# Kernel tuning notes

Hardware: AMD Instinct MI355X
Metric: run time of the kernel (lower is better)

The kernel has to match this reference:

```python
import jax, jax.numpy as jnp
import numpy as np

N, E, D, H, Z, HEADS = 20000, 160000, 3000, 512, 50, 3
EPS = 1e-5


def _bn(x, gamma, beta):
    # BatchNorm1d, training-mode stats (biased variance), eps=1e-5
    m = x.mean(axis=0)
    v = x.var(axis=0)
    return (x - m) * jax.lax.rsqrt(v + EPS) * gamma + beta


def _gat(x, src, dst, n, W, att_src, att_dst, bias, heads, c):
    # PyG GATConv, concat=False (mean over heads), negative_slope=0.2
    h = (x @ W).reshape(n, heads, c)                      # [N,H,C]
    a_s = (h * att_src).sum(-1)                           # [N,H]
    a_d = (h * att_dst).sum(-1)                           # [N,H]
    e = jax.nn.leaky_relu(a_s[src] + a_d[dst], 0.2)       # [Etot,H]
    e = e - jax.ops.segment_max(e, dst, num_segments=n)[dst]
    ex = jnp.exp(e)
    den = jax.ops.segment_sum(ex, dst, num_segments=n)[dst]
    alpha = ex / den                                      # segment softmax over incoming edges
    msg = h[src] * alpha[:, :, None]                      # [Etot,H,C]
    out = jax.ops.segment_sum(msg, dst, num_segments=n)   # [N,H,C]
    return out.mean(axis=1) + bias


def setup_inputs() -> dict:
    key = jax.random.key(0)
    ks = jax.random.split(key, 16)
    s = 0.05
    inp = {
        "x": jax.random.normal(ks[0], (N, D), dtype=jnp.float32),
        "edge_index": jax.random.randint(ks[1], (2, E), 0, N, dtype=jnp.int64),
        "W1": jax.random.normal(ks[2], (D, HEADS * H), dtype=jnp.float32) * s,
        "att_src1": jax.random.normal(ks[3], (HEADS, H), dtype=jnp.float32) * s,
        "att_dst1": jax.random.normal(ks[4], (HEADS, H), dtype=jnp.float32) * s,
        "b1": jnp.zeros((H,), jnp.float32),
        "bn1_g": jnp.ones((H,), jnp.float32),
        "bn1_b": jnp.zeros((H,), jnp.float32),
        "W2": jax.random.normal(ks[5], (H, HEADS * Z), dtype=jnp.float32) * s,
        "att_src2": jax.random.normal(ks[6], (HEADS, Z), dtype=jnp.float32) * s,
        "att_dst2": jax.random.normal(ks[7], (HEADS, Z), dtype=jnp.float32) * s,
        "b2": jnp.zeros((Z,), jnp.float32),
        "bn2_g": jnp.ones((Z,), jnp.float32),
        "bn2_b": jnp.zeros((Z,), jnp.float32),
        "lin1_w": jax.random.normal(ks[8], (H, Z), dtype=jnp.float32) * s,
        "lin1_b": jnp.zeros((H,), jnp.float32),
        "dbn_g": jnp.ones((H,), jnp.float32),
        "dbn_b": jnp.zeros((H,), jnp.float32),
        "lin2_w": jax.random.normal(ks[9], (D, H), dtype=jnp.float32) * s,
        "lin2_b": jnp.zeros((D,), jnp.float32),
    }
    return inp


def reference(x, edge_index, W1, att_src1, att_dst1, b1, bn1_g, bn1_b,
              W2, att_src2, att_dst2, b2, bn2_g, bn2_b,
              lin1_w, lin1_b, dbn_g, dbn_b, lin2_w, lin2_b):
    n = x.shape[0]
    loop = jnp.arange(n, dtype=edge_index.dtype)
    src = jnp.concatenate([edge_index[0], loop])  # add self-loops (PyG default)
    dst = jnp.concatenate([edge_index[1], loop])
    h = jax.nn.relu(_bn(_gat(x, src, dst, n, W1, att_src1, att_dst1, b1, HEADS, H), bn1_g, bn1_b))
    z = jax.nn.relu(_bn(_gat(h, src, dst, n, W2, att_src2, att_dst2, b2, HEADS, Z), bn2_g, bn2_b))
    d = jax.nn.relu(_bn(z @ lin1_w.T + lin1_b, dbn_g, dbn_b))
    out = jax.nn.relu(d @ lin2_w.T + lin2_b)
    return out
```

## Files before the change

### kernel.cpp

```cpp
#include <hip/hip_runtime.h>
#include <stdint.h>

typedef unsigned short u16;
typedef __attribute__((ext_vector_type(8))) short s16x8;
typedef __attribute__((ext_vector_type(4))) short s16x4;
typedef __attribute__((ext_vector_type(4))) float f32x4;

#define DEVFN static __device__ __forceinline__

static constexpr int NN = 20000;
static constexpr int EE = 160000;
static constexpr int ET = 180000;
static constexpr int DD = 3000;
static constexpr int HH = 512;
static constexpr int ZZ = 50;
static constexpr int C1 = 1536;
static constexpr int C2 = 150;
static constexpr int KA1 = 3008;
static constexpr int KP1 = 3072;

DEVFN u16 f2b(float f) {
  uint32_t u = __builtin_bit_cast(uint32_t, f);
  u += 0x7FFFu + ((u >> 16) & 1u);
  return (u16)(u >> 16);
}
DEVFN float b2f(u16 b) {
  uint32_t u = ((uint32_t)b) << 16;
  return __builtin_bit_cast(float, u);
}
DEVFN int edge_at(const void* ei, int mode32, long idx) {
  return mode32 ? ((const int*)ei)[idx] : (int)((const long long*)ei)[idx];
}

typedef __attribute__((address_space(1))) const unsigned int gas_uint;
typedef __attribute__((address_space(3))) unsigned int las_uint;
DEVFN void async16(const u16* g, u16* l) {
  __builtin_amdgcn_global_load_lds((gas_uint*)(uintptr_t)g,
                                   (las_uint*)(unsigned)(uintptr_t)l, 16, 0, 0);
}

DEVFN int sniff_mode(const void* ei, int* nzsh) {
  if (threadIdx.x == 0) *nzsh = 0;
  __syncthreads();
  const int* e32 = (const int*)ei;
  int loc = 0;
  for (int i = threadIdx.x; i < 1024; i += blockDim.x)
    if (e32[2 * i + 1] != 0) loc = 1;
  if (loc) atomicOr(nzsh, 1);
  __syncthreads();
  return *nzsh;
}

__global__ void k_deg(const void* ei, int* __restrict__ deg) {
  __shared__ int nz;
  int m = sniff_mode(ei, &nz);
  long i = (long)blockIdx.x * blockDim.x + threadIdx.x;
  long st = (long)gridDim.x * blockDim.x;
  for (; i < ET; i += st) {
    int d = (i < EE) ? edge_at(ei, m, EE + i) : (int)(i - EE);
    if ((unsigned)d < (unsigned)NN) atomicAdd(&deg[d], 1);
  }
}

__global__ void k_scan_blk(int* __restrict__ deg, int* __restrict__ rowptr,
                           int* __restrict__ bsum) {
  __shared__ int buf[256];
  int b = blockIdx.x, tid = threadIdx.x;
  int i = b * 256 + tid;
  buf[tid] = (i < NN) ? deg[i] : 0;
  if (i < NN) deg[i] = 0;
  __syncthreads();
  for (int off = 1; off < 256; off <<= 1) {
    int t = (tid >= off) ? buf[tid - off] : 0;
    __syncthreads();
    buf[tid] += t;
    __syncthreads();
  }
  if (i < NN) rowptr[i + 1] = buf[tid];
  if (tid == 255) bsum[b] = buf[255];
}
__global__ void k_scan_top(int* __restrict__ bsum, int nb) {
  __shared__ int buf[128];
  int tid = threadIdx.x;
  buf[tid] = (tid < nb) ? bsum[tid] : 0;
  __syncthreads();
  for (int off = 1; off < 128; off <<= 1) {
    int t = (tid >= off) ? buf[tid - off] : 0;
    __syncthreads();
    buf[tid] += t;
    __syncthreads();
  }
  if (tid < nb) bsum[tid] = buf[tid];
}
__global__ void k_scan_add(int* __restrict__ rowptr, const int* __restrict__ bsum) {
  int b = blockIdx.x, tid = threadIdx.x;
  int i = b * 256 + tid;
  if (i == 0) rowptr[0] = 0;
  if (b > 0 && i < NN) rowptr[i + 1] += bsum[b - 1];
}

__global__ void k_fill(const void* ei, const int* __restrict__ rowptr,
                       int* __restrict__ cursor, int* __restrict__ srcp) {
  __shared__ int nz;
  int m = sniff_mode(ei, &nz);
  long i = (long)blockIdx.x * blockDim.x + threadIdx.x;
  long st = (long)gridDim.x * blockDim.x;
  for (; i < ET; i += st) {
    int s, d;
    if (i < EE) { s = edge_at(ei, m, i); d = edge_at(ei, m, EE + i); }
    else { s = d = (int)(i - EE); }
    if ((unsigned)d < (unsigned)NN && (unsigned)s < (unsigned)NN) {
      int pos = atomicAdd(&cursor[d], 1);
      srcp[rowptr[d] + pos] = s;
    }
  }
}

__global__ void k_cvt_pad4(const float* __restrict__ in, u16* __restrict__ out,
                           int R, int Cin, int ldo) {
  int r = blockIdx.y;
  int c = (blockIdx.x * blockDim.x + threadIdx.x) * 4;
  if (c >= ldo) return;
  s16x4 o;
  const float* src = in + (size_t)r * Cin + c;
  if (r < R && c + 4 <= Cin && ((((size_t)r * Cin + c) & 3) == 0)) {
    f32x4 v = *(const f32x4*)src;
#pragma unroll
    for (int j = 0; j < 4; j++) o[j] = (short)f2b(v[j]);
  } else {
#pragma unroll
    for (int j = 0; j < 4; j++)
      o[j] = (short)((r < R && c + j < Cin) ? f2b(src[j]) : (u16)0);
  }
  *(s16x4*)(out + (size_t)r * ldo + c) = o;
}

__global__ void k_transpose_tile(const float* __restrict__ in, u16* __restrict__ out,
                                 int R, int Cc, int ldo) {
  __shared__ float t[32][33];
  int tx = threadIdx.x & 31, ty = threadIdx.x >> 5;
  int c0 = blockIdx.x * 32, r0 = blockIdx.y * 32;
#pragma unroll
  for (int j = 0; j < 4; j++) {
    int r = r0 + ty + j * 8, c = c0 + tx;
    t[ty + j * 8][tx] = (r < R && c < Cc) ? in[(size_t)r * Cc + c] : 0.f;
  }
  __syncthreads();
#pragma unroll
  for (int j = 0; j < 4; j++) {
    int c = c0 + ty + j * 8, r = r0 + tx;
    if (c < Cc && r < ldo) out[(size_t)c * ldo + r] = f2b(t[tx][ty + j * 8]);
  }
}

__global__ void k_transpose_cvt2(const float* __restrict__ in, u16* __restrict__ out,
                                 int R, int C, int Cp, int ldo) {
  long total = (long)Cp * ldo;
  long i = (long)blockIdx.x * blockDim.x + threadIdx.x;
  long st = (long)gridDim.x * blockDim.x;
  for (; i < total; i += st) {
    int c = (int)(i / ldo), r = (int)(i % ldo);
    out[i] = (c < C && r < R) ? f2b(in[(size_t)r * C + c]) : (u16)0;
  }
}

template<bool OUT_BF16, bool RELU>
__global__ __launch_bounds__(512, 2) void k_gemm8(
    const u16* __restrict__ Ag, const u16* __restrict__ Bg, void* __restrict__ Cg,
    const float* __restrict__ bias, int M, int Nn, int Kp, int lda, int ldb, int ldc) {
  __shared__ __align__(16) u16 As[2][256][64];
  __shared__ __align__(16) u16 Bs[2][256][64];
  int tid = threadIdx.x;
  int lane = tid & 63, wid = tid >> 6;
  int wm = wid >> 2, wn = wid & 3;
  int lr = lane & 15, lg = lane >> 4;
  int rx = lr & 7;

  int nwg = gridDim.x * gridDim.y;
  int wg = blockIdx.y * gridDim.x + blockIdx.x;
  int q = nwg >> 3, r = nwg & 7;
  int xcd = wg & 7, loc = wg >> 3;
  int swz = (xcd < r ? xcd * (q + 1) : r * (q + 1) + (xcd - r) * q) + loc;
  int m0 = (swz / gridDim.x) * 256, n0 = (swz % gridDim.x) * 256;

  int srow = tid >> 3;
  int schunk = ((tid & 7) ^ (srow & 7)) * 8;
  const u16* agp[4];
  const u16* bgp[4];
#pragma unroll
  for (int i = 0; i < 4; i++) {
    int ra = i * 64 + srow;
    int ga = m0 + ra; if (ga > M - 1) ga = M - 1;
    agp[i] = Ag + (size_t)ga * lda + schunk;
    bgp[i] = Bg + (size_t)(n0 + ra) * ldb + schunk;
  }
  u16* aB0 = &As[0][0][0]; u16* aB1 = &As[1][0][0];
  u16* bB0 = &Bs[0][0][0]; u16* bB1 = &Bs[1][0][0];

#define SA(cb, h, kt) do {                                                  \
    u16* d_ = ((cb) ? aB1 : aB0);                                           \
    async16(agp[2*(h)]   + (size_t)(kt)*64, d_ + (2*(h))*4096 + wid*512);   \
    async16(agp[2*(h)+1] + (size_t)(kt)*64, d_ + (2*(h)+1)*4096 + wid*512); \
  } while (0)
#define SB(cb, h, kt) do {                                                  \
    u16* d_ = ((cb) ? bB1 : bB0);                                           \
    async16(bgp[2*(h)]   + (size_t)(kt)*64, d_ + (2*(h))*4096 + wid*512);   \
    async16(bgp[2*(h)+1] + (size_t)(kt)*64, d_ + (2*(h)+1)*4096 + wid*512); \
  } while (0)
#define BARX() do { asm volatile("" ::: "memory");                          \
    __builtin_amdgcn_s_barrier(); asm volatile("" ::: "memory"); } while (0)
#define VMC4() asm volatile("s_waitcnt vmcnt(4)" ::: "memory")
#define RDA(dst, cb, mi, ks) dst = *(const s16x8*)&As[cb][wm*128+(mi)*16+lr][(((ks)*4+lg)^rx)*8]
#define RDB(dst, cb, ni, ks) dst = *(const s16x8*)&Bs[cb][wn*64+(ni)*16+lr][(((ks)*4+lg)^rx)*8]

  f32x4 acc[8][4];
#pragma unroll
  for (int mi = 0; mi < 8; mi++)
#pragma unroll
    for (int ni = 0; ni < 4; ni++) {
      acc[mi][ni][0] = 0.f; acc[mi][ni][1] = 0.f;
      acc[mi][ni][2] = 0.f; acc[mi][ni][3] = 0.f;
    }

  s16x8 bfr[2][4];
  s16x8 f0[4], f1[4];

#define RDB8(cb) do {                                                   \
    RDB(bfr[0][0], cb, 0, 0); RDB(bfr[0][1], cb, 1, 0);                 \
    RDB(bfr[0][2], cb, 2, 0); RDB(bfr[0][3], cb, 3, 0);                 \
    RDB(bfr[1][0], cb, 0, 1); RDB(bfr[1][1], cb, 1, 1);                 \
    RDB(bfr[1][2], cb, 2, 1); RDB(bfr[1][3], cb, 3, 1); } while (0)
#define RDAP(F, cb, P) do {                                             \
    RDA(F[0], cb, 2*(P), 0);   RDA(F[1], cb, 2*(P), 1);                 \
    RDA(F[2], cb, 2*(P)+1, 0); RDA(F[3], cb, 2*(P)+1, 1); } while (0)
#define DO_MFMA(P, F) do {                                              \
    _Pragma("unroll")                                                   \
    for (int ni_ = 0; ni_ < 4; ni_++) {                                 \
      acc[2*(P)][ni_]   = __builtin_amdgcn_mfma_f32_16x16x32_bf16(F[0], bfr[0][ni_], acc[2*(P)][ni_], 0, 0, 0);   \
      acc[2*(P)][ni_]   = __builtin_amdgcn_mfma_f32_16x16x32_bf16(F[1], bfr[1][ni_], acc[2*(P)][ni_], 0, 0, 0);   \
      acc[2*(P)+1][ni_] = __builtin_amdgcn_mfma_f32_16x16x32_bf16(F[2], bfr[0][ni_], acc[2*(P)+1][ni_], 0, 0, 0); \
      acc[2*(P)+1][ni_] = __builtin_amdgcn_mfma_f32_16x16x32_bf16(F[3], bfr[1][ni_], acc[2*(P)+1][ni_], 0, 0, 0); \
    } } while (0)

#define GROUP(cb, S1, S2, S3, S4) do {                                  \
    RDB8(cb); RDAP(f0, cb, 0);                                          \
    S1; BARX();                                                         \
    __builtin_amdgcn_s_setprio(1);                                      \
    RDAP(f1, cb, 1); DO_MFMA(0, f0);                                    \
    __builtin_amdgcn_s_setprio(0);                                      \
    S2; BARX();                                                         \
    __builtin_amdgcn_s_setprio(1);                                      \
    RDAP(f0, cb, 2); DO_MFMA(1, f1);                                    \
    __builtin_amdgcn_s_setprio(0);                                      \
    S3; BARX();                                                         \
    __builtin_amdgcn_s_setprio(1);                                      \
    RDAP(f1, cb, 3); DO_MFMA(2, f0);                                    \
    __builtin_amdgcn_s_setprio(0);                                      \
    S4; BARX();                                                         \
    __builtin_amdgcn_s_setprio(1);                                      \
    DO_MFMA(3, f1);                                                     \
    __builtin_amdgcn_s_setprio(0); VMC4(); BARX();                      \
  } while (0)

  int nt = Kp >> 6;
  SB(0, 0, 0); SB(0, 1, 0);
  SA(0, 0, 0); SA(0, 1, 0);
  { int k1 = 1 < nt ? 1 : nt - 1; SB(1, 0, k1); SB(1, 1, k1); }
  VMC4();
  BARX();

  for (int t = 0; t < nt; t += 2) {
    int t2 = (t + 2 < nt) ? t + 2 : nt - 1;
    int t3 = (t + 3 < nt) ? t + 3 : nt - 1;
    GROUP(0, SA(1, 0, t + 1), SA(1, 1, t + 1), SB(0, 0, t2), SB(0, 1, t2));
    GROUP(1, SA(0, 0, t2),    SA(0, 1, t2),    SB(1, 0, t3), SB(1, 1, t3));
  }
  asm volatile("s_waitcnt vmcnt(0)" ::: "memory");

#undef SA
#undef SB
#undef BARX
#undef VMC4
#undef RDA
#undef RDB
#undef RDB8
#undef RDAP
#undef DO_MFMA
#undef GROUP

#pragma unroll
  for (int mi = 0; mi < 8; mi++)
#pragma unroll
    for (int ni = 0; ni < 4; ni++) {
      int col = n0 + wn * 64 + ni * 16 + lr;
      if (col >= Nn) continue;
      float bv = bias ? bias[col] : 0.f;
#pragma unroll
      for (int j = 0; j < 4; j++) {
        int row = m0 + wm * 128 + mi * 16 + lg * 4 + j;
        if (row >= M) continue;
        float v = acc[mi][ni][j] + bv;
        if (RELU) v = v > 0.f ? v : 0.f;
        if (OUT_BF16) ((u16*)Cg)[(size_t)row * ldc + col] = f2b(v);
        else          ((float*)Cg)[(size_t)row * ldc + col] = v;
      }
    }
}

template<bool OUT_BF16, bool RELU>
__global__ __launch_bounds__(256) void k_gemm3(
    const u16* __restrict__ Ag, const u16* __restrict__ Bg, void* __restrict__ Cg,
    const float* __restrict__ bias, int M, int Nn, int Kp, int ld, int ldc) {
  __shared__ __align__(16) u16 As[2][128][64];
  __shared__ __align__(16) u16 Bs[2][128][64];
  int tid = threadIdx.x;
  int lane = tid & 63, wid = tid >> 6;
  int wm = wid >> 1, wn = wid & 1;
  int lr = lane & 15, lg = lane >> 4;

  int nwg = gridDim.x * gridDim.y;
  int wg = blockIdx.y * gridDim.x + blockIdx.x;
  int q = nwg >> 3, r = nwg & 7;
  int xcd = wg & 7, loc = wg >> 3;
  int swz = (xcd < r ? xcd * (q + 1) : r * (q + 1) + (xcd - r) * q) + loc;
  int m0 = (swz / gridDim.x) * 128, n0 = (swz % gridDim.x) * 128;

  int srow = lane >> 3;
  int skk = ((lane & 7) ^ srow) * 8;
  const u16* agp[4];
  const u16* bgp[4];
#pragma unroll
  for (int i = 0; i < 4; i++) {
    int ra = wid * 32 + i * 8 + srow;
    int ga = m0 + ra; if (ga > M - 1) ga = M - 1;
    agp[i] = Ag + (size_t)ga * ld + skk;
    bgp[i] = Bg + (size_t)(n0 + ra) * ld + skk;
  }

#define STAGE(bufi, kofs) do {                                   \
    u16* la_ = &As[bufi][0][0] + wid * 2048;                     \
    u16* lb_ = &Bs[bufi][0][0] + wid * 2048;                     \
    _Pragma("unroll")                                            \
    for (int i_ = 0; i_ < 4; i_++) {                             \
      async16(agp[i_] + (kofs), la_ + i_ * 512);                 \
      async16(bgp[i_] + (kofs), lb_ + i_ * 512);                 \
    }                                                            \
  } while (0)

  f32x4 acc[4][4];
#pragma unroll
  for (int mi = 0; mi < 4; mi++)
#pragma unroll
    for (int ni = 0; ni < 4; ni++) {
      acc[mi][ni][0] = 0.f; acc[mi][ni][1] = 0.f; acc[mi][ni][2] = 0.f; acc[mi][ni][3] = 0.f;
    }

  int rx = lr & 7;
  int NT = Kp >> 6;
  STAGE(0, 0);
  for (int t = 0; t < NT; t++) {
    int cur = t & 1;
    if (t + 1 < NT) {
      STAGE(cur ^ 1, (t + 1) * 64);
      asm volatile("s_waitcnt vmcnt(8)" ::: "memory");
    } else {
      asm volatile("s_waitcnt vmcnt(0)" ::: "memory");
    }
    __builtin_amdgcn_s_barrier();
    asm volatile("" ::: "memory");
#pragma unroll
    for (int ks = 0; ks < 2; ks++) {
      int ch = ((ks * 4 + lg) ^ rx) * 8;
      s16x8 a[4], b[4];
#pragma unroll
      for (int mi = 0; mi < 4; mi++)
        a[mi] = *(const s16x8*)&As[cur][wm * 64 + mi * 16 + lr][ch];
#pragma unroll
      for (int ni = 0; ni < 4; ni++)
        b[ni] = *(const s16x8*)&Bs[cur][wn * 64 + ni * 16 + lr][ch];
#pragma unroll
      for (int mi = 0; mi < 4; mi++)
#pragma unroll
        for (int ni = 0; ni < 4; ni++)
          acc[mi][ni] = __builtin_amdgcn_mfma_f32_16x16x32_bf16(a[mi], b[ni], acc[mi][ni], 0, 0, 0);
    }
    asm volatile("" ::: "memory");
    __builtin_amdgcn_s_barrier();
  }
#undef STAGE

#pragma unroll
  for (int mi = 0; mi < 4; mi++)
#pragma unroll
    for (int ni = 0; ni < 4; ni++) {
      int col = n0 + wn * 64 + ni * 16 + lr;
      if (col >= Nn) continue;
      float bv = bias ? bias[col] : 0.f;
#pragma unroll
      for (int j = 0; j < 4; j++) {
        int row = m0 + wm * 64 + mi * 16 + lg * 4 + j;
        if (row >= M) continue;
        float v = acc[mi][ni][j] + bv;
        if (RELU) v = v > 0.f ? v : 0.f;
        if (OUT_BF16) ((u16*)Cg)[(size_t)row * ldc + col] = f2b(v);
        else          ((float*)Cg)[(size_t)row * ldc + col] = v;
      }
    }
}

__global__ void k_attdot1b(const u16* __restrict__ h1b, const float* __restrict__ asrc,
                           const float* __restrict__ adst, float* __restrict__ as_,
                           float* __restrict__ ad_, float* __restrict__ z0,
                           float* __restrict__ z1) {
  int n = blockIdx.x;
  if (n == 0) {
    for (int i = threadIdx.x; i < HH; i += 192) { z0[i] = 0.f; z1[i] = 0.f; }
  }
  int hd = threadIdx.x >> 6, lane = threadIdx.x & 63;
  s16x8 h = *(const s16x8*)(h1b + (size_t)n * C1 + hd * 512 + lane * 8);
  const float* ap = asrc + hd * 512 + lane * 8;
  const float* dp = adst + hd * 512 + lane * 8;
  f32x4 a0 = *(const f32x4*)ap, a1 = *(const f32x4*)(ap + 4);
  f32x4 d0 = *(const f32x4*)dp, d1 = *(const f32x4*)(dp + 4);
  float ps = 0.f, pd = 0.f;
#pragma unroll
  for (int j = 0; j < 4; j++) {
    float hv = b2f((u16)h[j]);
    ps += hv * a0[j]; pd += hv * d0[j];
    float hw = b2f((u16)h[j + 4]);
    ps += hw * a1[j]; pd += hw * d1[j];
  }
  for (int off = 32; off; off >>= 1) { ps += __shfl_xor(ps, off); pd += __shfl_xor(pd, off); }
  if (lane == 0) { as_[3 * n + hd] = ps; ad_[3 * n + hd] = pd; }
}

__global__ void k_attdot2(const float* __restrict__ s2, const float* __restrict__ asrc,
                          const float* __restrict__ adst, float* __restrict__ as_,
                          float* __restrict__ ad_, float* __restrict__ z0,
                          float* __restrict__ z1, float* __restrict__ z2,
                          float* __restrict__ z3) {
  int n = blockIdx.x, tid = threadIdx.x;
  if (n == 0) {
    for (int i = tid; i < HH; i += 64) { z2[i] = 0.f; z3[i] = 0.f; }
    if (tid < 50) { z0[tid] = 0.f; z1[tid] = 0.f; }
  }
  for (int hd = 0; hd < 3; hd++) {
    float ps = 0.f, pd = 0.f;
    if (tid < 50) {
      float v = s2[(size_t)n * C2 + hd * 50 + tid];
      ps = v * asrc[hd * 50 + tid];
      pd = v * adst[hd * 50 + tid];
    }
    for (int off = 32; off; off >>= 1) { ps += __shfl_xor(ps, off); pd += __shfl_xor(pd, off); }
    if (tid == 0) { as_[3 * n + hd] = ps; ad_[3 * n + hd] = pd; }
  }
}

__global__ __launch_bounds__(192) void k_gat1(
    const u16* __restrict__ h1b, const float* __restrict__ as1,
    const float* __restrict__ ad1, const int* __restrict__ rowptr,
    const int* __restrict__ srcp, const float* __restrict__ bias,
    float* __restrict__ out) {
  int n = blockIdx.x, tid = threadIdx.x;
  __shared__ float sm[3], sden[3];
  __shared__ int s_src[128];
  __shared__ float s_alpha[128][3];
  __shared__ float part[3][512];
  int r0 = rowptr[n], deg = rowptr[n + 1] - r0;
  float adl[3] = {ad1[3 * n], ad1[3 * n + 1], ad1[3 * n + 2]};

  if (tid < 64) {
    float mx[3] = {-1e30f, -1e30f, -1e30f};
    for (int e = tid; e < deg; e += 64) {
      int s = srcp[r0 + e];
#pragma unroll
      for (int hd = 0; hd < 3; hd++) {
        float v = as1[3 * s + hd] + adl[hd];
        v = v > 0.f ? v : 0.2f * v;
        mx[hd] = fmaxf(mx[hd], v);
      }
    }
#pragma unroll
    for (int hd = 0; hd < 3; hd++)
      for (int off = 32; off; off >>= 1) mx[hd] = fmaxf(mx[hd], __shfl_xor(mx[hd], off));
    float sd[3] = {0.f, 0.f, 0.f};
    for (int e = tid; e < deg; e += 64) {
      int s = srcp[r0 + e];
#pragma unroll
      for (int hd = 0; hd < 3; hd++) {
        float v = as1[3 * s + hd] + adl[hd];
        v = v > 0.f ? v : 0.2f * v;
        sd[hd] += __expf(v - mx[hd]);
      }
    }
#pragma unroll
    for (int hd = 0; hd < 3; hd++)
      for (int off = 32; off; off >>= 1) sd[hd] += __shfl_xor(sd[hd], off);
    if (tid == 0) {
#pragma unroll
      for (int hd = 0; hd < 3; hd++) { sm[hd] = mx[hd]; sden[hd] = sd[hd]; }
    }
  }
  __syncthreads();

  int hd = tid >> 6, lane = tid & 63;
  float a[8];
#pragma unroll
  for (int j = 0; j < 8; j++) a[j] = 0.f;

  for (int base = 0; base < deg; base += 128) {
    int cnt = min(128, deg - base);
    if (tid < cnt) {
      int s = srcp[r0 + base + tid];
      s_src[tid] = s;
#pragma unroll
      for (int h2 = 0; h2 < 3; h2++) {
        float v = as1[3 * s + h2] + adl[h2];
        v = v > 0.f ? v : 0.2f * v;
        s_alpha[tid][h2] = __expf(v - sm[h2]) / sden[h2];
      }
    }
    __syncthreads();
    int e = 0;
    for (; e + 2 <= cnt; e += 2) {
      const u16* p0 = h1b + (size_t)s_src[e] * C1 + (hd << 9) + lane * 8;
      const u16* p1 = h1b + (size_t)s_src[e + 1] * C1 + (hd << 9) + lane * 8;
      s16x8 v0 = *(const s16x8*)p0;
      s16x8 v1 = *(const s16x8*)p1;
      float al0 = s_alpha[e][hd], al1 = s_alpha[e + 1][hd];
#pragma unroll
      for (int j = 0; j < 8; j++)
        a[j] += al0 * b2f((u16)v0[j]) + al1 * b2f((u16)v1[j]);
    }
    if (e < cnt) {
      const u16* p0 = h1b + (size_t)s_src[e] * C1 + (hd << 9) + lane * 8;
      s16x8 v0 = *(const s16x8*)p0;
      float al0 = s_alpha[e][hd];
#pragma unroll
      for (int j = 0; j < 8; j++) a[j] += al0 * b2f((u16)v0[j]);
    }
    __syncthreads();
  }

#pragma unroll
  for (int j = 0; j < 8; j++) part[hd][lane * 8 + j] = a[j];
  __syncthreads();
  if (tid < 128) {
    f32x4 p0 = *(const f32x4*)&part[0][tid * 4];
    f32x4 p1 = *(const f32x4*)&part[1][tid * 4];
    f32x4 p2 = *(const f32x4*)&part[2][tid * 4];
    f32x4 bv = *(const f32x4*)(bias + tid * 4);
    f32x4 o;
#pragma unroll
    for (int j = 0; j < 4; j++) o[j] = (p0[j] + p1[j] + p2[j]) * (1.f / 3.f) + bv[j];
    *(f32x4*)(out + (size_t)n * 512 + tid * 4) = o;
  }
}

__global__ void k_gat2(const float* __restrict__ s2, const float* __restrict__ as2,
                       const float* __restrict__ ad2, const int* __restrict__ rowptr,
                       const int* __restrict__ srcp, const float* __restrict__ bias,
                       float* __restrict__ z) {
  int n = blockIdx.x, tid = threadIdx.x;
  __shared__ int s_src[64];
  __shared__ float s_alpha[64][3];
  int r0 = rowptr[n], deg = rowptr[n + 1] - r0;
  float adl[3] = {ad2[3 * n], ad2[3 * n + 1], ad2[3 * n + 2]};

  float mx[3] = {-1e30f, -1e30f, -1e30f};
  for (int e = tid; e < deg; e += 64) {
    int s = srcp[r0 + e];
#pragma unroll
    for (int hd = 0; hd < 3; hd++) {
      float v = as2[3 * s + hd] + adl[hd];
      v = v > 0.f ? v : 0.2f * v;
      mx[hd] = fmaxf(mx[hd], v);
    }
  }
#pragma unroll
  for (int hd = 0; hd < 3; hd++)
    for (int off = 32; off; off >>= 1) mx[hd] = fmaxf(mx[hd], __shfl_xor(mx[hd], off));
  float sd[3] = {0.f, 0.f, 0.f};
  for (int e = tid; e < deg; e += 64) {
    int s = srcp[r0 + e];
#pragma unroll
    for (int hd = 0; hd < 3; hd++) {
      float v = as2[3 * s + hd] + adl[hd];
      v = v > 0.f ? v : 0.2f * v;
      sd[hd] += __expf(v - mx[hd]);
    }
  }
#pragma unroll
  for (int hd = 0; hd < 3; hd++)
    for (int off = 32; off; off >>= 1) sd[hd] += __shfl_xor(sd[hd], off);

  float acc = 0.f;
  for (int base = 0; base < deg; base += 64) {
    int cnt = min(64, deg - base);
    if (tid < cnt) {
      int s = srcp[r0 + base + tid];
      s_src[tid] = s;
#pragma unroll
      for (int hd = 0; hd < 3; hd++) {
        float v = as2[3 * s + hd] + adl[hd];
        v = v > 0.f ? v : 0.2f * v;
        s_alpha[tid][hd] = __expf(v - mx[hd]) / sd[hd];
      }
    }
    __syncthreads();
    if (tid < 50) {
      for (int e = 0; e < cnt; e++) {
        const float* row = s2 + (size_t)s_src[e] * C2;
#pragma unroll
        for (int hd = 0; hd < 3; hd++) acc += s_alpha[e][hd] * row[hd * 50 + tid];
      }
    }
    __syncthreads();
  }
  if (tid < 50) z[(size_t)n * ZZ + tid] = acc * (1.f / 3.f) + bias[tid];
}

__global__ void k_colstats3(const float* __restrict__ x, float* __restrict__ gsum,
                            float* __restrict__ gsq, long total, int C) {
  long i = (long)blockIdx.x * blockDim.x + threadIdx.x;
  long st = (long)gridDim.x * blockDim.x;
  int c = (int)(i % C);
  float s = 0.f, q = 0.f;
  for (; i < total; i += st) { float v = x[i]; s += v; q += v * v; }
  atomicAdd(&gsum[c], s);
  atomicAdd(&gsq[c], q);
}

__global__ void k_bnrelu4f(const float* __restrict__ x, const float* __restrict__ gsum,
                           const float* __restrict__ gsq, const float* __restrict__ g,
                           const float* __restrict__ bb, u16* __restrict__ out,
                           long total4, float invN) {
  long i = (long)blockIdx.x * blockDim.x + threadIdx.x;
  long st = (long)gridDim.x * blockDim.x;
  for (; i < total4; i += st) {
    long b = i * 4;
    int c = (int)(b & 511);
    f32x4 v = *(const f32x4*)(x + b);
    f32x4 s = *(const f32x4*)(gsum + c);
    f32x4 qv = *(const f32x4*)(gsq + c);
    f32x4 gg = *(const f32x4*)(g + c);
    f32x4 bv = *(const f32x4*)(bb + c);
    s16x4 o;
#pragma unroll
    for (int j = 0; j < 4; j++) {
      float m = s[j] * invN;
      float var = qv[j] * invN - m * m;
      float sc = gg[j] * rsqrtf(var + 1e-5f);
      float r = (v[j] - m) * sc + bv[j];
      r = r > 0.f ? r : 0.f;
      o[j] = (short)f2b(r);
    }
    *(s16x4*)(out + b) = o;
  }
}

__global__ void k_bnrelu_padf(const float* __restrict__ x, const float* __restrict__ gsum,
                              const float* __restrict__ gsq, const float* __restrict__ g,
                              const float* __restrict__ bb, u16* __restrict__ out) {
  int i = blockIdx.x * blockDim.x + threadIdx.x;
  if (i >= NN * 64) return;
  int c = i & 63, r = i >> 6;
  float v = 0.f;
  if (c < 50) {
    float m = gsum[c] * (1.0f / NN);
    float var = gsq[c] * (1.0f / NN) - m * m;
    float sc = g[c] * rsqrtf(var + 1e-5f);
    v = (x[r * 50 + c] - m) * sc + bb[c];
    v = v > 0.f ? v : 0.f;
  }
  out[i] = f2b(v);
}

extern "C" void kernel_launch(void* const* d_in, const int* in_sizes, int n_in,
                              void* d_out, int out_size, void* d_ws, size_t ws_size,
                              hipStream_t stream) {
  (void)in_sizes; (void)n_in; (void)out_size;
  const float* x     = (const float*)d_in[0];
  const void*  ei    = d_in[1];
  const float* W1    = (const float*)d_in[2];
  const float* asrc1 = (const float*)d_in[3];
  const float* adst1 = (const float*)d_in[4];
  const float* b1    = (const float*)d_in[5];
  const float* bn1g  = (const float*)d_in[6];
  const float* bn1b  = (const float*)d_in[7];
  const float* W2    = (const float*)d_in[8];
  const float* asrc2 = (const float*)d_in[9];
  const float* adst2 = (const float*)d_in[10];
  const float* b2    = (const float*)d_in[11];
  const float* bn2g  = (const float*)d_in[12];
  const float* bn2b  = (const float*)d_in[13];
  const float* l1w   = (const float*)d_in[14];
  const float* l1b   = (const float*)d_in[15];
  const float* dbng  = (const float*)d_in[16];
  const float* dbnb  = (const float*)d_in[17];
  const float* l2w   = (const float*)d_in[18];
  const float* l2b   = (const float*)d_in[19];
  float* out = (float*)d_out;
  char* ws = (char*)d_ws;

  size_t off = 0;
  auto alloc = [&](size_t b) { size_t r = off; off += (b + 255) & ~(size_t)255; return r; };
  const size_t oXB  = alloc(120320000);
  const size_t oH1  = alloc(61440000);
  const size_t oW1T = alloc((size_t)C1 * KP1 * 2);
  const size_t oAS1 = alloc((size_t)NN * 12), oAD1 = alloc((size_t)NN * 12);
  const size_t oAS2 = alloc((size_t)NN * 12), oAD2 = alloc((size_t)NN * 12);
  const size_t oRP  = alloc((size_t)(NN + 1) * 4);
  const size_t oDEG = alloc((size_t)NN * 4);
  const size_t oSRC = alloc((size_t)ET * 4);
  const size_t oBSUM = alloc(512);
  const size_t oS1 = alloc(2048), oQ1 = alloc(2048);
  const size_t oS2 = alloc(2048), oQ2 = alloc(2048);
  const size_t oS3 = alloc(2048), oQ3 = alloc(2048);
  if (ws_size < off) return;

  u16*   xb   = (u16*)(ws + oXB);
  float* g1   = (float*)(ws + oXB);
  u16*   h2b  = (u16*)(ws + oXB + 40960000);
  float* s2   = (float*)(ws + oXB + 61440000);
  float* zf   = (float*)(ws + oXB + 73440000);
  u16*   zb   = (u16*)(ws + oXB + 77440000);
  u16*   w2T  = (u16*)(ws + oXB + 80000000);
  u16*   l1wT = (u16*)(ws + oXB + 80262400);
  u16*   l2wT = (u16*)(ws + oXB + 80328192);
  float* dbuf = (float*)(ws + oXB);
  u16*   h1b  = (u16*)(ws + oH1);
  u16*   db   = (u16*)(ws + oH1);
  u16*   w1T  = (u16*)(ws + oW1T);
  int* bsum   = (int*)(ws + oBSUM);
  int* deg    = (int*)(ws + oDEG);
  int* rowptr = (int*)(ws + oRP);
  int* srcp   = (int*)(ws + oSRC);
  float *as1 = (float*)(ws + oAS1), *ad1 = (float*)(ws + oAD1);
  float *as2 = (float*)(ws + oAS2), *ad2 = (float*)(ws + oAD2);
  float *sum1 = (float*)(ws + oS1), *sq1 = (float*)(ws + oQ1);
  float *sum2 = (float*)(ws + oS2), *sq2 = (float*)(ws + oQ2);
  float *sum3 = (float*)(ws + oS3), *sq3 = (float*)(ws + oQ3);

  hipMemsetAsync(deg, 0, (size_t)NN * 4, stream);
  k_deg<<<512, 256, 0, stream>>>(ei, deg);
  k_scan_blk<<<79, 256, 0, stream>>>(deg, rowptr, bsum);
  k_scan_top<<<1, 128, 0, stream>>>(bsum, 79);
  k_scan_add<<<79, 256, 0, stream>>>(rowptr, bsum);
  k_fill<<<512, 256, 0, stream>>>(ei, rowptr, deg, srcp);

  k_cvt_pad4<<<dim3(3, NN), 256, 0, stream>>>(x, xb, NN, DD, KA1);
  k_transpose_tile<<<dim3(C1 / 32, KP1 / 32), 256, 0, stream>>>(W1, w1T, DD, C1, KP1);
  k_gemm8<true, false><<<dim3(6, 79), 512, 0, stream>>>(xb, w1T, h1b, nullptr,
                                                        NN, C1, KP1, KA1, KP1, C1);
  k_attdot1b<<<NN, 192, 0, stream>>>(h1b, asrc1, adst1, as1, ad1, sum1, sq1);
  k_gat1<<<NN, 192, 0, stream>>>(h1b, as1, ad1, rowptr, srcp, b1, g1);
  k_colstats3<<<512, 256, 0, stream>>>(g1, sum1, sq1, (long)NN * HH, HH);
  k_bnrelu4f<<<2048, 256, 0, stream>>>(g1, sum1, sq1, bn1g, bn1b, h2b,
                                       (long)NN * HH / 4, 1.0f / NN);

  k_transpose_cvt2<<<256, 256, 0, stream>>>(W2, w2T, HH, C2, 256, HH);
  k_gemm3<false, false><<<dim3(2, 157), 256, 0, stream>>>(h2b, w2T, s2, nullptr,
                                                          NN, C2, HH, HH, C2);
  k_attdot2<<<NN, 64, 0, stream>>>(s2, asrc2, adst2, as2, ad2, sum2, sq2, sum3, sq3);
  k_gat2<<<NN, 64, 0, stream>>>(s2, as2, ad2, rowptr, srcp, b2, zf);
  k_colstats3<<<25, 256, 0, stream>>>(zf, sum2, sq2, (long)NN * ZZ, ZZ);
  k_bnrelu_padf<<<5000, 256, 0, stream>>>(zf, sum2, sq2, bn2g, bn2b, zb);

  k_cvt_pad4<<<dim3(1, HH), 256, 0, stream>>>(l1w, l1wT, HH, ZZ, 64);
  k_gemm3<false, false><<<dim3(4, 157), 256, 0, stream>>>(zb, l1wT, dbuf, l1b,
                                                          NN, HH, 64, 64, HH);
  k_colstats3<<<512, 256, 0, stream>>>(dbuf, sum3, sq3, (long)NN * HH, HH);
  k_bnrelu4f<<<2048, 256, 0, stream>>>(dbuf, sum3, sq3, dbng, dbnb, db,
                                       (long)NN * HH / 4, 1.0f / NN);
  k_cvt_pad4<<<dim3(1, 3072), 256, 0, stream>>>(l2w, l2wT, DD, HH, HH);
  k_gemm8<false, true><<<dim3(12, 79), 512, 0, stream>>>(db, l2wT, out, l2b,
                                                         NN, DD, 512, HH, HH, DD);
}
```

Before: 716.2 us.

## Fuse fp32-to-bf16 conversion of x into first GEMM's A-tile loads

Removes the separate pass that converts and pads x (20000x3000 fp32) to bf16. The first GEMM now loads fp32 A directly through registers, converts to bf16 and writes it to LDS, with zero-fill past the real K. This saves one full write and one full read of the bf16 copy of x. In exchange, the A path loses async global-to-LDS copies, reads twice the bytes per tile, and adds conversion ALU work and register pressure inside the MFMA loop.

```diff
diff --git a/kernel.cpp b/kernel.cpp
--- a/kernel.cpp
+++ b/kernel.cpp
@@ -16,7 +16,6 @@
 static constexpr int ZZ = 50;
 static constexpr int C1 = 1536;
 static constexpr int C2 = 150;
-static constexpr int KA1 = 3008;
 static constexpr int KP1 = 3072;
 
 DEVFN u16 f2b(float f) {
@@ -164,10 +163,11 @@
   }
 }
 
-template<bool OUT_BF16, bool RELU>
+template<bool OUT_BF16, bool RELU, bool A_F32>
 __global__ __launch_bounds__(512, 2) void k_gemm8(
     const u16* __restrict__ Ag, const u16* __restrict__ Bg, void* __restrict__ Cg,
-    const float* __restrict__ bias, int M, int Nn, int Kp, int lda, int ldb, int ldc) {
+    const float* __restrict__ bias, int M, int Nn, int Kp, int lda, int ldb, int ldc,
+    int Kreal) {
   __shared__ __align__(16) u16 As[2][256][64];
   __shared__ __align__(16) u16 Bs[2][256][64];
   int tid = threadIdx.x;
@@ -186,13 +186,16 @@
   int srow = tid >> 3;
   int schunk = ((tid & 7) ^ (srow & 7)) * 8;
   const u16* agp[4];
+  const float* agf[4];
   const u16* bgp[4];
+  const float* Af = (const float*)Ag;
 #pragma unroll
   for (int i = 0; i < 4; i++) {
-    int ra = i * 64 + srow;
-    int ga = m0 + ra; if (ga > M - 1) ga = M - 1;
+    int ra_ = i * 64 + srow;
+    int ga = m0 + ra_; if (ga > M - 1) ga = M - 1;
     agp[i] = Ag + (size_t)ga * lda + schunk;
-    bgp[i] = Bg + (size_t)(n0 + ra) * ldb + schunk;
+    agf[i] = Af + (size_t)ga * lda + schunk;
+    bgp[i] = Bg + (size_t)(n0 + ra_) * ldb + schunk;
   }
   u16* aB0 = &As[0][0][0]; u16* aB1 = &As[1][0][0];
   u16* bB0 = &Bs[0][0][0]; u16* bB1 = &Bs[1][0][0];
@@ -224,6 +227,37 @@
 
   s16x8 bfr[2][4];
   s16x8 f0[4], f1[4];
+  s16x8 fs[4];
+  f32x4 ra[4];
+
+#define LOADA_F(h, kt) do {                                             \
+    int kk_ = (kt) * 64 + schunk;                                       \
+    _Pragma("unroll")                                                   \
+    for (int j_ = 0; j_ < 2; j_++) {                                    \
+      const float* p_ = agf[2*(h)+j_] + (size_t)(kt) * 64;              \
+      if (kk_ + 8 <= Kreal) {                                           \
+        ra[2*j_]   = *(const f32x4*)p_;                                 \
+        ra[2*j_+1] = *(const f32x4*)(p_ + 4);                           \
+      } else {                                                          \
+        _Pragma("unroll")                                               \
+        for (int e_ = 0; e_ < 4; e_++) {                                \
+          ra[2*j_][e_]   = (kk_ + e_     < Kreal) ? p_[e_]     : 0.f;   \
+          ra[2*j_+1][e_] = (kk_ + 4 + e_ < Kreal) ? p_[e_ + 4] : 0.f;   \
+        }                                                               \
+      }                                                                 \
+    } } while (0)
+#define CVTW_F(buf, h) do {                                             \
+    u16* d_ = ((buf) ? aB1 : aB0);                                      \
+    _Pragma("unroll")                                                   \
+    for (int j_ = 0; j_ < 2; j_++) {                                    \
+      s16x8 o_;                                                         \
+      _Pragma("unroll")                                                 \
+      for (int e_ = 0; e_ < 4; e_++) {                                  \
+        o_[e_]     = (short)f2b(ra[2*j_][e_]);                          \
+        o_[e_ + 4] = (short)f2b(ra[2*j_+1][e_]);                        \
+      }                                                                 \
+      *(s16x8*)(d_ + (2*(h)+j_)*4096 + tid*8) = o_;                     \
+    } } while (0)
 
 #define RDB8(cb) do {                                                   \
     RDB(bfr[0][0], cb, 0, 0); RDB(bfr[0][1], cb, 1, 0);                 \
@@ -262,18 +296,58 @@
     __builtin_amdgcn_s_setprio(0); VMC4(); BARX();                      \
   } while (0)
 
+#define GROUPF(cb, ktA, ktAn, S3, S4) do {                              \
+    RDB8(cb);                                                           \
+    CVTW_F((cb) ^ 1, 0);                                                \
+    LOADA_F(1, ktA);                                                    \
+    RDAP(fs, cb, 0);                                                    \
+    BARX();                                                             \
+    __builtin_amdgcn_s_setprio(1); DO_MFMA(0, fs);                      \
+    __builtin_amdgcn_s_setprio(0);                                      \
+    CVTW_F((cb) ^ 1, 1);                                                \
+    RDAP(fs, cb, 1);                                                    \
+    BARX();                                                             \
+    __builtin_amdgcn_s_setprio(1); DO_MFMA(1, fs);                      \
+    __builtin_amdgcn_s_setprio(0);                                      \
+    S3; RDAP(fs, cb, 2);                                                \
+    BARX();                                                             \
+    __builtin_amdgcn_s_setprio(1); DO_MFMA(2, fs);                      \
+    __builtin_amdgcn_s_setprio(0);                                      \
+    S4; LOADA_F(0, ktAn);                                               \
+    RDAP(fs, cb, 3);                                                    \
+    BARX();                                                             \
+    __builtin_amdgcn_s_setprio(1); DO_MFMA(3, fs);                      \
+    __builtin_amdgcn_s_setprio(0); BARX();                              \
+  } while (0)
+
   int nt = Kp >> 6;
-  SB(0, 0, 0); SB(0, 1, 0);
-  SA(0, 0, 0); SA(0, 1, 0);
-  { int k1 = 1 < nt ? 1 : nt - 1; SB(1, 0, k1); SB(1, 1, k1); }
-  VMC4();
-  BARX();
-
-  for (int t = 0; t < nt; t += 2) {
-    int t2 = (t + 2 < nt) ? t + 2 : nt - 1;
-    int t3 = (t + 3 < nt) ? t + 3 : nt - 1;
-    GROUP(0, SA(1, 0, t + 1), SA(1, 1, t + 1), SB(0, 0, t2), SB(0, 1, t2));
-    GROUP(1, SA(0, 0, t2),    SA(0, 1, t2),    SB(1, 0, t3), SB(1, 1, t3));
+  if constexpr (A_F32) {
+    SB(0, 0, 0); SB(0, 1, 0);
+    LOADA_F(0, 0); CVTW_F(0, 0);
+    LOADA_F(1, 0); CVTW_F(0, 1);
+    int k1 = 1 < nt ? 1 : nt - 1;
+    SB(1, 0, k1); SB(1, 1, k1);
+    LOADA_F(0, k1);
+    asm volatile("s_waitcnt lgkmcnt(0)" ::: "memory");
+    BARX();
+    for (int t = 0; t < nt; t += 2) {
+      int t2 = (t + 2 < nt) ? t + 2 : nt - 1;
+      int t3 = (t + 3 < nt) ? t + 3 : nt - 1;
+      GROUPF(0, t + 1, t2, SB(0, 0, t2), SB(0, 1, t2));
+      GROUPF(1, t2, t3, SB(1, 0, t3), SB(1, 1, t3));
+    }
+  } else {
+    SB(0, 0, 0); SB(0, 1, 0);
+    SA(0, 0, 0); SA(0, 1, 0);
+    { int k1 = 1 < nt ? 1 : nt - 1; SB(1, 0, k1); SB(1, 1, k1); }
+    VMC4();
+    BARX();
+    for (int t = 0; t < nt; t += 2) {
+      int t2 = (t + 2 < nt) ? t + 2 : nt - 1;
+      int t3 = (t + 3 < nt) ? t + 3 : nt - 1;
+      GROUP(0, SA(1, 0, t + 1), SA(1, 1, t + 1), SB(0, 0, t2), SB(0, 1, t2));
+      GROUP(1, SA(0, 0, t2),    SA(0, 1, t2),    SB(1, 0, t3), SB(1, 1, t3));
+    }
   }
   asm volatile("s_waitcnt vmcnt(0)" ::: "memory");
 
@@ -287,6 +361,9 @@
 #undef RDAP
 #undef DO_MFMA
 #undef GROUP
+#undef GROUPF
+#undef LOADA_F
+#undef CVTW_F
 
 #pragma unroll
   for (int mi = 0; mi < 8; mi++)
@@ -719,7 +796,6 @@
   const size_t oS3 = alloc(2048), oQ3 = alloc(2048);
   if (ws_size < off) return;
 
-  u16*   xb   = (u16*)(ws + oXB);
   float* g1   = (float*)(ws + oXB);
   u16*   h2b  = (u16*)(ws + oXB + 40960000);
   float* s2   = (float*)(ws + oXB + 61440000);
@@ -749,10 +825,9 @@
   k_scan_add<<<79, 256, 0, stream>>>(rowptr, bsum);
   k_fill<<<512, 256, 0, stream>>>(ei, rowptr, deg, srcp);
 
-  k_cvt_pad4<<<dim3(3, NN), 256, 0, stream>>>(x, xb, NN, DD, KA1);
   k_transpose_tile<<<dim3(C1 / 32, KP1 / 32), 256, 0, stream>>>(W1, w1T, DD, C1, KP1);
-  k_gemm8<true, false><<<dim3(6, 79), 512, 0, stream>>>(xb, w1T, h1b, nullptr,
-                                                        NN, C1, KP1, KA1, KP1, C1);
+  k_gemm8<true, false, true><<<dim3(6, 79), 512, 0, stream>>>(
+      (const u16*)x, w1T, h1b, nullptr, NN, C1, KP1, DD, KP1, C1, DD);
   k_attdot1b<<<NN, 192, 0, stream>>>(h1b, asrc1, adst1, as1, ad1, sum1, sq1);
   k_gat1<<<NN, 192, 0, stream>>>(h1b, as1, ad1, rowptr, srcp, b1, g1);
   k_colstats3<<<512, 256, 0, stream>>>(g1, sum1, sq1, (long)NN * HH, HH);
@@ -774,6 +849,6 @@
   k_bnrelu4f<<<2048, 256, 0, stream>>>(dbuf, sum3, sq3, dbng, dbnb, db,
                                        (long)NN * HH / 4, 1.0f / NN);
   k_cvt_pad4<<<dim3(1, 3072), 256, 0, stream>>>(l2w, l2wT, DD, HH, HH);
-  k_gemm8<false, true><<<dim3(12, 79), 512, 0, stream>>>(db, l2wT, out, l2b,
-                                                         NN, DD, 512, HH, HH, DD);
-}
+  k_gemm8<false, true, false><<<dim3(12, 79), 512, 0, stream>>>(
+      db, l2wT, out, l2b, NN, DD, 512, HH, HH, DD, 512);
+}
```

After: 778.4 us. +8.7%, slower.
